# Kernel optimization log

Measured on AMD Instinct MI355X. Metric: run time of the kernel, lower is better.

## Reference

```python
import jax, jax.numpy as jnp
import numpy as np

NEG = -1.0e9


def setup_inputs() -> dict:
    key = jax.random.key(0)
    ks = jax.random.split(key, 8)
    B, L, D = 4, 2048, 1024
    s = 1.0 / np.sqrt(D)
    return {
        "x": jax.random.normal(ks[0], (B, L, D), dtype=jnp.float32),
        "Wq": jax.random.normal(ks[1], (D, D), dtype=jnp.float32) * s,
        "bq": jax.random.normal(ks[2], (D,), dtype=jnp.float32) * 0.02,
        "Wk": jax.random.normal(ks[3], (D, D), dtype=jnp.float32) * s,
        "bk": jax.random.normal(ks[4], (D,), dtype=jnp.float32) * 0.02,
        "Wv": jax.random.normal(ks[5], (D, D), dtype=jnp.float32) * s,
        "bv": jax.random.normal(ks[6], (D,), dtype=jnp.float32) * 0.02,
        "lengths": jax.random.randint(ks[7], (B,), 1, 2048, dtype=jnp.int32),
    }


def reference(x, Wq, bq, Wk, bk, Wv, bv, lengths):
    # x: [B, L, D]; single-head self-attention with causal + length additive masks
    B, L, D = x.shape
    q = x @ Wq + bq  # [B, L, D]
    k = x @ Wk + bk
    v = x @ Wv + bv
    scale = 1.0 / jnp.sqrt(jnp.asarray(D, dtype=x.dtype))
    att = jnp.einsum("bid,bjd->bij", q, k) * scale  # [B, L, L]
    idx = jnp.arange(L)
    causal = jnp.where(idx[None, :] > idx[:, None], NEG, 0.0).astype(x.dtype)  # [L, L]
    # length mask: NEG where j >= len[b] or i >= len[b]
    invalid = (idx[None, :] >= lengths[:, None])  # [B, L]
    lenmask = jnp.where(invalid[:, :, None] | invalid[:, None, :], NEG, 0.0).astype(x.dtype)
    att = att + causal[None, :, :] + lenmask
    att = jax.nn.softmax(att, axis=-1)
    return jnp.einsum("bij,bjd->bid", att, v)
```

## Files before the change

kernel.cpp:

```cpp
#include <hip/hip_runtime.h>

#define NEGV (-1.0e9f)

typedef __bf16 bf16_t;
typedef __bf16 bf16x8 __attribute__((ext_vector_type(8)));
typedef __bf16 bf16x4 __attribute__((ext_vector_type(4)));
typedef float  f32x4  __attribute__((ext_vector_type(4)));

__device__ __forceinline__ void gld16(const void* g, void* l) {
    __builtin_amdgcn_global_load_lds(
        (const __attribute__((address_space(1))) void*)g,
        (__attribute__((address_space(3))) void*)l, 16, 0, 0);
}


#define MMR(AF, IB)                                                                        \
    acc[IB][0] = __builtin_amdgcn_mfma_f32_16x16x32_bf16(AF, b0, acc[IB][0], 0, 0, 0);     \
    acc[IB][1] = __builtin_amdgcn_mfma_f32_16x16x32_bf16(AF, b1, acc[IB][1], 0, 0, 0);     \
    acc[IB][2] = __builtin_amdgcn_mfma_f32_16x16x32_bf16(AF, b2, acc[IB][2], 0, 0, 0);     \
    acc[IB][3] = __builtin_amdgcn_mfma_f32_16x16x32_bf16(AF, b3, acc[IB][3], 0, 0, 0)

__device__ __forceinline__ void ml256x256(
    const bf16_t* __restrict__ A, const bf16_t* __restrict__ B,
    int ldA, int ldB, int nkt, char* smem, int tid, f32x4 acc[8][4])
{
    const int w = tid >> 6, lane = tid & 63;
    const int wm = w & 1, wn = w >> 1;
    const int l16 = lane & 15, quad = lane >> 4;

    const int g0 = 2 * (tid >> 3) + ((tid >> 2) & 1);
    const int c0 = ((tid & 3) ^ ((tid >> 3) & 3)) * 8;
    const bf16_t* pa0 = A + (size_t)g0 * ldA + c0;
    const bf16_t* pa1 = pa0 + (size_t)128 * ldA;
    const bf16_t* pb0 = B + (size_t)g0 * ldB + c0;
    const bf16_t* pb1 = pb0 + (size_t)128 * ldB;
    char* const stA = smem + (w << 10);
    char* const stB = smem + 16384 + (w << 10);

    const int rowo = (l16 >> 1) * 128 + (l16 & 1) * 64 + ((quad ^ ((l16 >> 1) & 3)) << 4);
    const char* rdA = smem + (wm << 13) + rowo;
    const char* rdB = smem + 16384 + (wn << 12) + rowo;

#define STG6(BO) do { gld16(pa0, stA + (BO)); gld16(pa1, stA + (BO) + 8192);   \
                      gld16(pb0, stB + (BO)); gld16(pb1, stB + (BO) + 8192);   \
                      pa0 += 32; pa1 += 32; pb0 += 32; pb1 += 32; } while (0)

    STG6(0);
    if (nkt > 1) {
        STG6(32768);
        asm volatile("s_waitcnt vmcnt(4)" ::: "memory");
    } else {
        asm volatile("s_waitcnt vmcnt(0)" ::: "memory");
    }
    __builtin_amdgcn_s_barrier();

    int ro = 0, so = 65536;
    for (int kt = 0; kt < nkt; ++kt) {
        const char* ra = rdA + ro;
        const char* rb = rdB + ro;
        bf16x8 a0 = *(const bf16x8*)(ra);
        bf16x8 a1 = *(const bf16x8*)(ra + 1024);
        bf16x8 a2 = *(const bf16x8*)(ra + 2048);
        bf16x8 a3 = *(const bf16x8*)(ra + 3072);
        bf16x8 b0 = *(const bf16x8*)(rb);
        bf16x8 b1 = *(const bf16x8*)(rb + 1024);
        bf16x8 b2 = *(const bf16x8*)(rb + 2048);
        bf16x8 b3 = *(const bf16x8*)(rb + 3072);
        bf16x8 a4 = *(const bf16x8*)(ra + 4096);
        bf16x8 a5 = *(const bf16x8*)(ra + 5120);
        bf16x8 a6 = *(const bf16x8*)(ra + 6144);
        bf16x8 a7 = *(const bf16x8*)(ra + 7168);
        const bool st = (kt + 2) < nkt;
        if (st) STG6(so);
        asm volatile("s_waitcnt lgkmcnt(4)" ::: "memory");
        __builtin_amdgcn_sched_barrier(0);
        __builtin_amdgcn_s_setprio(1);
        MMR(a0, 0); MMR(a1, 1); MMR(a2, 2); MMR(a3, 3);
        __builtin_amdgcn_s_setprio(0);
        asm volatile("s_waitcnt lgkmcnt(0)" ::: "memory");
        __builtin_amdgcn_sched_barrier(0);
        __builtin_amdgcn_s_setprio(1);
        MMR(a4, 4); MMR(a5, 5); MMR(a6, 6); MMR(a7, 7);
        __builtin_amdgcn_s_setprio(0);
        if (st) asm volatile("s_waitcnt vmcnt(4)" ::: "memory");
        else    asm volatile("s_waitcnt vmcnt(0)" ::: "memory");
        __builtin_amdgcn_s_barrier();
        ro = (ro == 65536) ? 0 : (ro + 32768);
        so = (so == 65536) ? 0 : (so + 32768);
    }
#undef STG6
}

__device__ __forceinline__ void ml256x128(
    const bf16_t* __restrict__ A, const bf16_t* __restrict__ B,
    int ldA, int ldB, int nkt, char* smem, int tid, f32x4 acc[4][4])
{
    const int w = tid >> 6, lane = tid & 63;
    const int wm = w & 3, wn = w >> 2;
    const int l16 = lane & 15, quad = lane >> 4;

    const int g0 = 2 * (tid >> 3) + ((tid >> 2) & 1);
    const int c0 = ((tid & 3) ^ ((tid >> 3) & 3)) * 8;
    const bf16_t* pa0 = A + (size_t)g0 * ldA + c0;
    const bf16_t* pa1 = pa0 + (size_t)128 * ldA;
    const bf16_t* pb0 = B + (size_t)g0 * ldB + c0;
    char* const stA = smem + (w << 10);
    char* const stB = smem + 16384 + (w << 10);

    const int rowo = (l16 >> 1) * 128 + (l16 & 1) * 64 + ((quad ^ ((l16 >> 1) & 3)) << 4);
    const char* rdA = smem + (wm << 12) + rowo;
    const char* rdB = smem + 16384 + (wn << 12) + rowo;

#define STG3(BO) do { gld16(pa0, stA + (BO)); gld16(pa1, stA + (BO) + 8192);   \
                      gld16(pb0, stB + (BO));                                  \
                      pa0 += 32; pa1 += 32; pb0 += 32; } while (0)

    STG3(0);
    if (nkt > 1) {
        STG3(24576);
        asm volatile("s_waitcnt vmcnt(3)" ::: "memory");
    } else {
        asm volatile("s_waitcnt vmcnt(0)" ::: "memory");
    }
    __builtin_amdgcn_s_barrier();

    int ro = 0, so = 49152;
    for (int kt = 0; kt < nkt; ++kt) {
        const char* ra = rdA + ro;
        const char* rb = rdB + ro;
        bf16x8 a0 = *(const bf16x8*)(ra);
        bf16x8 a1 = *(const bf16x8*)(ra + 1024);
        bf16x8 a2 = *(const bf16x8*)(ra + 2048);
        bf16x8 a3 = *(const bf16x8*)(ra + 3072);
        bf16x8 b0 = *(const bf16x8*)(rb);
        bf16x8 b1 = *(const bf16x8*)(rb + 1024);
        bf16x8 b2 = *(const bf16x8*)(rb + 2048);
        bf16x8 b3 = *(const bf16x8*)(rb + 3072);
        const bool st = (kt + 2) < nkt;
        if (st) STG3(so);
        asm volatile("s_waitcnt lgkmcnt(0)" ::: "memory");
        __builtin_amdgcn_sched_barrier(0);
        __builtin_amdgcn_s_setprio(1);
        MMR(a0, 0); MMR(a1, 1); MMR(a2, 2); MMR(a3, 3);
        __builtin_amdgcn_s_setprio(0);
        if (st) asm volatile("s_waitcnt vmcnt(3)" ::: "memory");
        else    asm volatile("s_waitcnt vmcnt(0)" ::: "memory");
        __builtin_amdgcn_s_barrier();
        ro = (ro == 49152) ? 0 : (ro + 24576);
        so = (so == 49152) ? 0 : (so + 24576);
    }
#undef STG3
}

__global__ __launch_bounds__(256)
void convert_x_kernel(const float* __restrict__ x, bf16_t* __restrict__ xb)
{
    const size_t i = ((size_t)blockIdx.x * 256 + threadIdx.x) * 8;
    float4 a = *(const float4*)&x[i];
    float4 b = *(const float4*)&x[i + 4];
    bf16x8 o;
    o[0] = (bf16_t)a.x; o[1] = (bf16_t)a.y; o[2] = (bf16_t)a.z; o[3] = (bf16_t)a.w;
    o[4] = (bf16_t)b.x; o[5] = (bf16_t)b.y; o[6] = (bf16_t)b.z; o[7] = (bf16_t)b.w;
    *(bf16x8*)&xb[i] = o;
}

__global__ __launch_bounds__(256)
void transpose_w_kernel(const float* __restrict__ W0, const float* __restrict__ W1,
                        const float* __restrict__ W2, bf16_t* __restrict__ WT)
{
    __shared__ float t[32][33];
    const float* W = (blockIdx.z == 0) ? W0 : (blockIdx.z == 1) ? W1 : W2;
    bf16_t* WTz = WT + (size_t)blockIdx.z * 1024 * 1024;
    const int k0 = blockIdx.y * 32, n0 = blockIdx.x * 32;
    const int r = threadIdx.x >> 3, c4 = (threadIdx.x & 7) * 4;
    float4 v = *(const float4*)&W[(size_t)(k0 + r) * 1024 + n0 + c4];
    t[r][c4 + 0] = v.x; t[r][c4 + 1] = v.y; t[r][c4 + 2] = v.z; t[r][c4 + 3] = v.w;
    __syncthreads();
    bf16x4 o;
#pragma unroll
    for (int j = 0; j < 4; ++j) o[j] = (bf16_t)t[c4 + j][r];
    *(bf16x4*)&WTz[(size_t)(n0 + r) * 1024 + k0 + c4] = o;
}

__global__ __launch_bounds__(512, 2)
void gemm_qk256(const bf16_t* __restrict__ A, const bf16_t* __restrict__ Bt,
                const float* __restrict__ bq, const float* __restrict__ bk,
                bf16_t* __restrict__ C, int N, int Kd)
{
    __shared__ __align__(16) char smem[98304];
    int bid = blockIdx.y * 8 + blockIdx.x;
    bid = (bid & 7) * 32 + (bid >> 3);
    const int n0 = (bid & 7) * 256;
    const int m0 = (bid >> 3) * 256;
    const int tid = threadIdx.x;

    f32x4 acc[8][4];
#pragma unroll
    for (int i = 0; i < 8; ++i)
#pragma unroll
        for (int j = 0; j < 4; ++j) acc[i][j] = (f32x4)(0.0f);

    ml256x256(A + (size_t)m0 * Kd, Bt + (size_t)n0 * Kd, Kd, Kd, Kd >> 5,
              smem, tid, acc);

    const int w = tid >> 6, lane = tid & 63;
    const int wm = w & 1, wn = w >> 1, quad = lane >> 4, l16 = lane & 15;
#pragma unroll
    for (int j = 0; j < 4; ++j) {
        const int col = n0 + wn * 64 + j * 16 + l16;
        const float bval = (col < 1024) ? bq[col] : bk[col - 1024];
#pragma unroll
        for (int i = 0; i < 8; ++i) {
            const int row = m0 + wm * 128 + i * 16 + quad * 4;
#pragma unroll
            for (int r = 0; r < 4; ++r)
                C[(size_t)(row + r) * N + col] = (bf16_t)(acc[i][j][r] + bval);
        }
    }
}

__global__ __launch_bounds__(512, 2)
void gemm_vt256(const bf16_t* __restrict__ WvT, const bf16_t* __restrict__ xb,
                const float* __restrict__ bv, bf16_t* __restrict__ VT,
                int N, int Kd)
{
    __shared__ __align__(16) char smem[73728];
    int bid = blockIdx.y * 64 + blockIdx.x;
    bid = (bid & 7) * 32 + (bid >> 3);
    const int m0 = (bid >> 6) * 256;
    const int n0 = (bid & 63) * 128;
    const int tid = threadIdx.x;

    f32x4 acc[4][4];
#pragma unroll
    for (int i = 0; i < 4; ++i)
#pragma unroll
        for (int j = 0; j < 4; ++j) acc[i][j] = (f32x4)(0.0f);

    ml256x128(WvT + (size_t)m0 * Kd, xb + (size_t)n0 * Kd, Kd, Kd, Kd >> 5,
              smem, tid, acc);

    const int w = tid >> 6, lane = tid & 63;
    const int wm = w & 3, wn = w >> 2, quad = lane >> 4, l16 = lane & 15;
#pragma unroll
    for (int i = 0; i < 4; ++i) {
        const int row = m0 + wm * 64 + i * 16 + quad * 4;
#pragma unroll
        for (int r = 0; r < 4; ++r) {
            const float bval = bv[row + r];
#pragma unroll
            for (int j = 0; j < 4; ++j) {
                const int col = n0 + wn * 64 + j * 16 + l16;
                VT[(size_t)(row + r) * N + col] = (bf16_t)(acc[i][j][r] + bval);
            }
        }
    }
}

__global__ __launch_bounds__(512, 2)
void scores256(const bf16_t* __restrict__ Q, const bf16_t* __restrict__ K,
               int ldq, const int* __restrict__ lengths,
               float* __restrict__ S, int L, int Dd, float alpha)
{
    __shared__ __align__(16) char smem[98304];
    const int b = blockIdx.z;
    const int len = lengths[b];
    int it = 0;
    while ((it + 1) * (it + 2) / 2 <= (int)blockIdx.x) ++it;
    const int jt = blockIdx.x - it * (it + 1) / 2;
    const int m0 = it * 256, n0 = jt * 256;
    float* Sb = S + (size_t)b * L * L;
    const int tid = threadIdx.x;

    f32x4 acc[8][4];
#pragma unroll
    for (int i = 0; i < 8; ++i)
#pragma unroll
        for (int j = 0; j < 4; ++j) acc[i][j] = (f32x4)(0.0f);

    const bf16_t* Qb = Q + (size_t)b * L * ldq + (size_t)m0 * ldq;
    const bf16_t* Kb = K + (size_t)b * L * ldq + (size_t)n0 * ldq;
    ml256x256(Qb, Kb, ldq, ldq, Dd >> 5, smem, tid, acc);

    const int w = tid >> 6, lane = tid & 63;
    const int wm = w & 1, wn = w >> 1, quad = lane >> 4, l16 = lane & 15;
#pragma unroll
    for (int i = 0; i < 8; ++i) {
#pragma unroll
        for (int j = 0; j < 4; ++j) {
            const int col = n0 + wn * 64 + j * 16 + l16;
#pragma unroll
            for (int r = 0; r < 4; ++r) {
                const int row = m0 + wm * 128 + i * 16 + quad * 4 + r;
                float s = acc[i][j][r] * alpha;
                if (col > row) s += NEGV;
                if (row >= len || col >= len) s += NEGV;
                Sb[(size_t)row * L + col] = s;
            }
        }
    }
}

__global__ __launch_bounds__(256)
void softmax_kernel(const float* __restrict__ S, bf16_t* __restrict__ P,
                    int L, int ldp)
{
    __shared__ float red[8];
    const int i = blockIdx.x;
    const int bound  = ((i >> 7) + 1) << 7;
    const int bound2 = ((i >> 8) + 1) << 8;
    const float* row = S + ((size_t)blockIdx.y * L + i) * L;
    bf16_t* prow = P + ((size_t)blockIdx.y * L + i) * ldp;
    const int t = threadIdx.x;
    const int w = t >> 6, lane = t & 63;
    const int j8 = t * 8;
    const bool act = j8 < bound;

    float v[8];
    float m = -3.0e38f;
    if (act) {
        float4 a = *(const float4*)&row[j8];
        float4 b = *(const float4*)&row[j8 + 4];
        v[0] = a.x; v[1] = a.y; v[2] = a.z; v[3] = a.w;
        v[4] = b.x; v[5] = b.y; v[6] = b.z; v[7] = b.w;
#pragma unroll
        for (int j = 0; j < 8; ++j) m = fmaxf(m, v[j]);
    }
#pragma unroll
    for (int off = 32; off > 0; off >>= 1) m = fmaxf(m, __shfl_down(m, off, 64));
    if (lane == 0) red[w] = m;
    __syncthreads();
    m = fmaxf(fmaxf(red[0], red[1]), fmaxf(red[2], red[3]));

    float s = 0.f;
    if (act) {
#pragma unroll
        for (int j = 0; j < 8; ++j) {
            v[j] = __expf(v[j] - m);
            s += v[j];
        }
    }
#pragma unroll
    for (int off = 32; off > 0; off >>= 1) s += __shfl_down(s, off, 64);
    if (lane == 0) red[4 + w] = s;
    __syncthreads();
    s = red[4] + red[5] + red[6] + red[7];

    if (act) {
        const float inv = 1.0f / s;
        bf16x8 o;
#pragma unroll
        for (int j = 0; j < 8; ++j) o[j] = (bf16_t)(v[j] * inv);
        *(bf16x8*)&prow[j8] = o;
    } else if (j8 < bound2) {
        bf16x8 z;
#pragma unroll
        for (int j = 0; j < 8; ++j) z[j] = (bf16_t)0.0f;
        *(bf16x8*)&prow[j8] = z;
    }
}

__global__ __launch_bounds__(512, 2)
void pv256(const bf16_t* __restrict__ P, int ldp,
           const bf16_t* __restrict__ VT, int ldv,
           float* __restrict__ O, int L, int Dd)
{
    __shared__ __align__(16) char smem[73728];
    const int b = blockIdx.z;
    int bid = blockIdx.y * 8 + blockIdx.x;
    bid = (bid & 7) * 8 + (bid >> 3);
    const int mt = 7 - (bid >> 3);
    const int m0 = mt * 256, n0 = (bid & 7) * 128;
    const int tid = threadIdx.x;

    f32x4 acc[4][4];
#pragma unroll
    for (int i = 0; i < 4; ++i)
#pragma unroll
        for (int j = 0; j < 4; ++j) acc[i][j] = (f32x4)(0.0f);

    const int nkt = (m0 + 256) >> 5;
    const bf16_t* Pb = P + (size_t)b * L * ldp + (size_t)m0 * ldp;
    const bf16_t* Vb = VT + (size_t)b * L + (size_t)n0 * ldv;
    ml256x128(Pb, Vb, ldp, ldv, nkt, smem, tid, acc);

    float* Ob = O + (size_t)b * L * Dd;
    const int w = tid >> 6, lane = tid & 63;
    const int wm = w & 3, wn = w >> 2, quad = lane >> 4, l16 = lane & 15;
#pragma unroll
    for (int i = 0; i < 4; ++i) {
        const int row = m0 + wm * 64 + i * 16 + quad * 4;
#pragma unroll
        for (int j = 0; j < 4; ++j) {
            const int col = n0 + wn * 64 + j * 16 + l16;
#pragma unroll
            for (int r = 0; r < 4; ++r)
                Ob[(size_t)(row + r) * Dd + col] = acc[i][j][r];
        }
    }
}

extern "C" void kernel_launch(void* const* d_in, const int* in_sizes, int n_in,
                              void* d_out, int out_size, void* d_ws, size_t ws_size,
                              hipStream_t stream)
{
    const float* x  = (const float*)d_in[0];
    const float* Wq = (const float*)d_in[1];
    const float* bq = (const float*)d_in[2];
    const float* Wk = (const float*)d_in[3];
    const float* bk = (const float*)d_in[4];
    const float* Wv = (const float*)d_in[5];
    const float* bv = (const float*)d_in[6];
    const int*  len = (const int*)d_in[7];
    float* out = (float*)d_out;

    const int B = 4, L = 2048, D = 1024;
    const int M = B * L;
    const int N2 = 2 * D;

    bf16_t* xb = (bf16_t*)d_ws;
    bf16_t* WT = xb + (size_t)M * D;
    bf16_t* QK = WT + (size_t)3 * D * D;
    bf16_t* VT = QK + (size_t)M * N2;
    float*  S  = (float*)(VT + (size_t)D * M);
    bf16_t* P  = QK;

    convert_x_kernel<<<(M * D) / 2048, 256, 0, stream>>>(x, xb);

    transpose_w_kernel<<<dim3(32, 32, 3), 256, 0, stream>>>(Wq, Wk, Wv, WT);

    gemm_qk256<<<dim3(8, 32), 512, 0, stream>>>(xb, WT, bq, bk, QK, N2, D);

    gemm_vt256<<<dim3(64, 4), 512, 0, stream>>>(
        WT + (size_t)2 * D * D, xb, bv, VT, M, D);

    scores256<<<dim3(36, 1, B), 512, 0, stream>>>(
        QK, QK + 1024, N2, len, S, L, D, 0.03125f);

    softmax_kernel<<<dim3(L, B), 256, 0, stream>>>(S, P, L, N2);

    pv256<<<dim3(8, 8, 4), 512, 0, stream>>>(P, N2, VT, M, out, L, D);
}
```

Before: 244.0 us.

## Fuse partial softmax into scores epilogue and rescale P chunks in PV load

The scores kernel now computes per-64-column chunk max and exp-sum in its epilogue and stores unnormalized exponentials as bf16 instead of fp32 logits. A small finalize kernel combines the chunk statistics into per-chunk scale factors. The PV kernel loads U through registers, multiplies each element by its chunk scale, and writes it to LDS. This replaces the full softmax pass over an fp32 LxL matrix and halves score storage traffic, at the cost of register-staged A loads in the PV pipeline instead of direct global-to-LDS loads, plus added epilogue shuffles.

```diff
diff --git a/kernel.cpp b/kernel.cpp
--- a/kernel.cpp
+++ b/kernel.cpp
@@ -152,6 +152,94 @@
 #undef STG3
 }
 
+__device__ __forceinline__ bf16x8 scale8(bf16x8 u, float c) {
+    bf16x8 o;
+#pragma unroll
+    for (int j = 0; j < 8; ++j) o[j] = (bf16_t)((float)u[j] * c);
+    return o;
+}
+
+__device__ __forceinline__ void ml_pv(
+    const bf16_t* __restrict__ A, const float* __restrict__ scA,
+    const bf16_t* __restrict__ B,
+    int ldA, int ldB, int nkt, char* smem, int tid, f32x4 acc[4][4])
+{
+    const int w = tid >> 6, lane = tid & 63;
+    const int wm = w & 3, wn = w >> 2;
+    const int l16 = lane & 15, quad = lane >> 4;
+
+    const int g0 = 2 * (tid >> 3) + ((tid >> 2) & 1);
+    const int c0 = ((tid & 3) ^ ((tid >> 3) & 3)) * 8;
+    const bf16_t* pa0 = A + (size_t)g0 * ldA + c0;
+    const bf16_t* pa1 = pa0 + (size_t)128 * ldA;
+    const bf16_t* pb0 = B + (size_t)g0 * ldB + c0;
+    const float* sc0 = scA + g0 * 32;
+    const float* sc1 = sc0 + 128 * 32;
+
+    char* const stB = smem + 16384 + (w << 10);
+    char* const wA0 = smem + tid * 16;
+    char* const wA1 = smem + 8192 + tid * 16;
+
+    const int rowo = (l16 >> 1) * 128 + (l16 & 1) * 64 + ((quad ^ ((l16 >> 1) & 3)) << 4);
+    const char* rdA = smem + (wm << 12) + rowo;
+    const char* rdB = smem + 16384 + (wn << 12) + rowo;
+
+    {
+        bf16x8 x00 = *(const bf16x8*)(pa0);
+        bf16x8 x01 = *(const bf16x8*)(pa1);
+        bf16x8 x10 = *(const bf16x8*)(pa0 + 32);
+        bf16x8 x11 = *(const bf16x8*)(pa1 + 32);
+        gld16(pb0, stB + 0);     pb0 += 32;
+        gld16(pb0, stB + 24576); pb0 += 32;
+        const float c00 = sc0[c0 >> 6],        c01 = sc1[c0 >> 6];
+        const float c10 = sc0[(32 + c0) >> 6], c11 = sc1[(32 + c0) >> 6];
+        *(bf16x8*)(wA0)         = scale8(x00, c00);
+        *(bf16x8*)(wA1)         = scale8(x01, c01);
+        *(bf16x8*)(wA0 + 24576) = scale8(x10, c10);
+        *(bf16x8*)(wA1 + 24576) = scale8(x11, c11);
+        asm volatile("s_waitcnt vmcnt(0) lgkmcnt(0)" ::: "memory");
+        __builtin_amdgcn_s_barrier();
+    }
+
+    int ro = 0, so = 49152;
+    for (int kt = 0; kt < nkt; ++kt) {
+        const bool st = (kt + 2) < nkt;
+        bf16x8 x0, x1; float ca0 = 0.f, ca1 = 0.f;
+        if (st) {
+            x0 = *(const bf16x8*)(pa0 + (size_t)(kt + 2) * 32);
+            x1 = *(const bf16x8*)(pa1 + (size_t)(kt + 2) * 32);
+            const int ch = ((kt + 2) * 32 + c0) >> 6;
+            ca0 = sc0[ch]; ca1 = sc1[ch];
+            gld16(pb0, stB + so); pb0 += 32;
+        }
+        const char* ra = rdA + ro;
+        const char* rb = rdB + ro;
+        bf16x8 a0 = *(const bf16x8*)(ra);
+        bf16x8 a1 = *(const bf16x8*)(ra + 1024);
+        bf16x8 a2 = *(const bf16x8*)(ra + 2048);
+        bf16x8 a3 = *(const bf16x8*)(ra + 3072);
+        bf16x8 b0 = *(const bf16x8*)(rb);
+        bf16x8 b1 = *(const bf16x8*)(rb + 1024);
+        bf16x8 b2 = *(const bf16x8*)(rb + 2048);
+        bf16x8 b3 = *(const bf16x8*)(rb + 3072);
+        asm volatile("s_waitcnt lgkmcnt(0)" ::: "memory");
+        __builtin_amdgcn_sched_barrier(0);
+        __builtin_amdgcn_s_setprio(1);
+        MMR(a0, 0); MMR(a1, 1); MMR(a2, 2); MMR(a3, 3);
+        __builtin_amdgcn_s_setprio(0);
+        if (st) {
+            *(bf16x8*)(wA0 + so) = scale8(x0, ca0);
+            *(bf16x8*)(wA1 + so) = scale8(x1, ca1);
+        } else {
+            asm volatile("s_waitcnt vmcnt(0)" ::: "memory");
+        }
+        asm volatile("s_waitcnt lgkmcnt(0)" ::: "memory");
+        __builtin_amdgcn_s_barrier();
+        ro = (ro == 49152) ? 0 : (ro + 24576);
+        so = (so == 49152) ? 0 : (so + 24576);
+    }
+}
+
 __global__ __launch_bounds__(256)
 void convert_x_kernel(const float* __restrict__ x, bf16_t* __restrict__ xb)
 {
@@ -260,7 +348,8 @@
 __global__ __launch_bounds__(512, 2)
 void scores256(const bf16_t* __restrict__ Q, const bf16_t* __restrict__ K,
                int ldq, const int* __restrict__ lengths,
-               float* __restrict__ S, int L, int Dd, float alpha)
+               bf16_t* __restrict__ U, float2* __restrict__ stats,
+               int L, int Dd, float alpha)
 {
     __shared__ __align__(16) char smem[98304];
     const int b = blockIdx.z;
@@ -269,7 +358,6 @@
     while ((it + 1) * (it + 2) / 2 <= (int)blockIdx.x) ++it;
     const int jt = blockIdx.x - it * (it + 1) / 2;
     const int m0 = it * 256, n0 = jt * 256;
-    float* Sb = S + (size_t)b * L * L;
     const int tid = threadIdx.x;
 
     f32x4 acc[8][4];
@@ -284,84 +372,74 @@
 
     const int w = tid >> 6, lane = tid & 63;
     const int wm = w & 1, wn = w >> 1, quad = lane >> 4, l16 = lane & 15;
+    bf16_t* Ub = U + (size_t)b * L * L;
+    float2* strow = stats + (size_t)b * L * 32;
+    const int chnk = (n0 >> 6) + wn;
 #pragma unroll
     for (int i = 0; i < 8; ++i) {
 #pragma unroll
-        for (int j = 0; j < 4; ++j) {
-            const int col = n0 + wn * 64 + j * 16 + l16;
-#pragma unroll
-            for (int r = 0; r < 4; ++r) {
-                const int row = m0 + wm * 128 + i * 16 + quad * 4 + r;
-                float s = acc[i][j][r] * alpha;
-                if (col > row) s += NEGV;
-                if (row >= len || col >= len) s += NEGV;
-                Sb[(size_t)row * L + col] = s;
+        for (int r = 0; r < 4; ++r) {
+            const int row = m0 + wm * 128 + i * 16 + quad * 4 + r;
+            float sv[4];
+#pragma unroll
+            for (int j = 0; j < 4; ++j) {
+                const int col = n0 + wn * 64 + j * 16 + l16;
+                float v = acc[i][j][r] * alpha;
+                if (col > row) v += NEGV;
+                if (row >= len || col >= len) v += NEGV;
+                sv[j] = v;
             }
+            float m = fmaxf(fmaxf(sv[0], sv[1]), fmaxf(sv[2], sv[3]));
+            m = fmaxf(m, __shfl_xor(m, 1, 64));
+            m = fmaxf(m, __shfl_xor(m, 2, 64));
+            m = fmaxf(m, __shfl_xor(m, 4, 64));
+            m = fmaxf(m, __shfl_xor(m, 8, 64));
+            float ssum = 0.f;
+#pragma unroll
+            for (int j = 0; j < 4; ++j) {
+                sv[j] = __expf(sv[j] - m);
+                ssum += sv[j];
+            }
+            ssum += __shfl_xor(ssum, 1, 64);
+            ssum += __shfl_xor(ssum, 2, 64);
+            ssum += __shfl_xor(ssum, 4, 64);
+            ssum += __shfl_xor(ssum, 8, 64);
+#pragma unroll
+            for (int j = 0; j < 4; ++j)
+                Ub[(size_t)row * L + n0 + wn * 64 + j * 16 + l16] = (bf16_t)sv[j];
+            if (l16 == 0) strow[(size_t)row * 32 + chnk] = make_float2(m, ssum);
         }
     }
 }
 
 __global__ __launch_bounds__(256)
-void softmax_kernel(const float* __restrict__ S, bf16_t* __restrict__ P,
-                    int L, int ldp)
-{
-    __shared__ float red[8];
-    const int i = blockIdx.x;
-    const int bound  = ((i >> 7) + 1) << 7;
-    const int bound2 = ((i >> 8) + 1) << 8;
-    const float* row = S + ((size_t)blockIdx.y * L + i) * L;
-    bf16_t* prow = P + ((size_t)blockIdx.y * L + i) * ldp;
+void sm_finalize(const float2* __restrict__ stats, float* __restrict__ scale, int L)
+{
     const int t = threadIdx.x;
-    const int w = t >> 6, lane = t & 63;
-    const int j8 = t * 8;
-    const bool act = j8 < bound;
-
-    float v[8];
-    float m = -3.0e38f;
-    if (act) {
-        float4 a = *(const float4*)&row[j8];
-        float4 b = *(const float4*)&row[j8 + 4];
-        v[0] = a.x; v[1] = a.y; v[2] = a.z; v[3] = a.w;
-        v[4] = b.x; v[5] = b.y; v[6] = b.z; v[7] = b.w;
-#pragma unroll
-        for (int j = 0; j < 8; ++j) m = fmaxf(m, v[j]);
-    }
-#pragma unroll
-    for (int off = 32; off > 0; off >>= 1) m = fmaxf(m, __shfl_down(m, off, 64));
-    if (lane == 0) red[w] = m;
-    __syncthreads();
-    m = fmaxf(fmaxf(red[0], red[1]), fmaxf(red[2], red[3]));
-
-    float s = 0.f;
-    if (act) {
-#pragma unroll
-        for (int j = 0; j < 8; ++j) {
-            v[j] = __expf(v[j] - m);
-            s += v[j];
-        }
-    }
-#pragma unroll
-    for (int off = 32; off > 0; off >>= 1) s += __shfl_down(s, off, 64);
-    if (lane == 0) red[4 + w] = s;
-    __syncthreads();
-    s = red[4] + red[5] + red[6] + red[7];
-
-    if (act) {
-        const float inv = 1.0f / s;
-        bf16x8 o;
-#pragma unroll
-        for (int j = 0; j < 8; ++j) o[j] = (bf16_t)(v[j] * inv);
-        *(bf16x8*)&prow[j8] = o;
-    } else if (j8 < bound2) {
-        bf16x8 z;
-#pragma unroll
-        for (int j = 0; j < 8; ++j) z[j] = (bf16_t)0.0f;
-        *(bf16x8*)&prow[j8] = z;
-    }
+    const int c = t & 31;
+    const int row = blockIdx.x * 8 + (t >> 5);
+    const size_t base = ((size_t)blockIdx.y * L + row) * 32;
+    const int nch = ((row >> 8) + 1) << 2;
+    float m_c = -3.0e38f, s_c = 0.f;
+    if (c < nch) { float2 st = stats[base + c]; m_c = st.x; s_c = st.y; }
+    float M = m_c;
+    M = fmaxf(M, __shfl_xor(M, 1, 64));
+    M = fmaxf(M, __shfl_xor(M, 2, 64));
+    M = fmaxf(M, __shfl_xor(M, 4, 64));
+    M = fmaxf(M, __shfl_xor(M, 8, 64));
+    M = fmaxf(M, __shfl_xor(M, 16, 64));
+    const float e = __expf(m_c - M);
+    float d = s_c * e;
+    d += __shfl_xor(d, 1, 64);
+    d += __shfl_xor(d, 2, 64);
+    d += __shfl_xor(d, 4, 64);
+    d += __shfl_xor(d, 8, 64);
+    d += __shfl_xor(d, 16, 64);
+    if (c < nch) scale[base + c] = e / d;
 }
 
 __global__ __launch_bounds__(512, 2)
-void pv256(const bf16_t* __restrict__ P, int ldp,
+void pv256(const bf16_t* __restrict__ U, int ldp, const float* __restrict__ scale,
            const bf16_t* __restrict__ VT, int ldv,
            float* __restrict__ O, int L, int Dd)
 {
@@ -380,9 +458,10 @@
         for (int j = 0; j < 4; ++j) acc[i][j] = (f32x4)(0.0f);
 
     const int nkt = (m0 + 256) >> 5;
-    const bf16_t* Pb = P + (size_t)b * L * ldp + (size_t)m0 * ldp;
+    const bf16_t* Pb = U + (size_t)b * L * ldp + (size_t)m0 * ldp;
+    const float* scA = scale + ((size_t)b * L + m0) * 32;
     const bf16_t* Vb = VT + (size_t)b * L + (size_t)n0 * ldv;
-    ml256x128(Pb, Vb, ldp, ldv, nkt, smem, tid, acc);
+    ml_pv(Pb, scA, Vb, ldp, ldv, nkt, smem, tid, acc);
 
     float* Ob = O + (size_t)b * L * Dd;
     const int w = tid >> 6, lane = tid & 63;
@@ -422,8 +501,9 @@
     bf16_t* WT = xb + (size_t)M * D;
     bf16_t* QK = WT + (size_t)3 * D * D;
     bf16_t* VT = QK + (size_t)M * N2;
-    float*  S  = (float*)(VT + (size_t)D * M);
-    bf16_t* P  = QK;
+    bf16_t* U  = VT + (size_t)D * M;
+    float2* stats = (float2*)(U + (size_t)B * L * L);
+    float*  scale = (float*)(stats + (size_t)B * L * 32);
 
     convert_x_kernel<<<(M * D) / 2048, 256, 0, stream>>>(x, xb);
 
@@ -435,9 +515,9 @@
         WT + (size_t)2 * D * D, xb, bv, VT, M, D);
 
     scores256<<<dim3(36, 1, B), 512, 0, stream>>>(
-        QK, QK + 1024, N2, len, S, L, D, 0.03125f);
-
-    softmax_kernel<<<dim3(L, B), 256, 0, stream>>>(S, P, L, N2);
-
-    pv256<<<dim3(8, 8, 4), 512, 0, stream>>>(P, N2, VT, M, out, L, D);
-}
+        QK, QK + 1024, N2, len, U, stats, L, D, 0.03125f);
+
+    sm_finalize<<<dim3(L / 8, B), 256, 0, stream>>>(stats, scale, L);
+
+    pv256<<<dim3(8, 8, 4), 512, 0, stream>>>(U, L, scale, VT, M, out, L, D);
+}
```

After: 275.4 us. 1.13x slower.

## Fuse partial softmax into scores kernel, store bf16 exps with per-chunk stats

Applied to the files above, without the earlier changes.

The scores kernel now computes per-row, per-64-column-chunk max and exp-sum in registers and writes unnormalized bf16 exponentials plus float2 stats, instead of writing fp32 scores. A small finalize kernel combines the chunk stats into per-chunk scale factors and rescales the bf16 row in place before the PV GEMM reads it. This halves score-matrix traffic and removes the separate max and sum passes over fp32 data. In exchange it adds an extra bf16 rounding before rescaling, and P now lives in a new buffer with leading dimension L instead of reusing the QK buffer.

```diff
diff --git a/kernel.cpp b/kernel.cpp
--- a/kernel.cpp
+++ b/kernel.cpp
@@ -260,7 +260,8 @@
 __global__ __launch_bounds__(512, 2)
 void scores256(const bf16_t* __restrict__ Q, const bf16_t* __restrict__ K,
                int ldq, const int* __restrict__ lengths,
-               float* __restrict__ S, int L, int Dd, float alpha)
+               bf16_t* __restrict__ U, float2* __restrict__ stats,
+               int L, int Dd, float alpha)
 {
     __shared__ __align__(16) char smem[98304];
     const int b = blockIdx.z;
@@ -269,7 +270,6 @@
     while ((it + 1) * (it + 2) / 2 <= (int)blockIdx.x) ++it;
     const int jt = blockIdx.x - it * (it + 1) / 2;
     const int m0 = it * 256, n0 = jt * 256;
-    float* Sb = S + (size_t)b * L * L;
     const int tid = threadIdx.x;
 
     f32x4 acc[8][4];
@@ -284,79 +284,86 @@
 
     const int w = tid >> 6, lane = tid & 63;
     const int wm = w & 1, wn = w >> 1, quad = lane >> 4, l16 = lane & 15;
+    bf16_t* Ub = U + (size_t)b * L * L;
+    float2* strow = stats + (size_t)b * L * 32;
+    const int chnk = (n0 >> 6) + wn;
 #pragma unroll
     for (int i = 0; i < 8; ++i) {
 #pragma unroll
-        for (int j = 0; j < 4; ++j) {
-            const int col = n0 + wn * 64 + j * 16 + l16;
-#pragma unroll
-            for (int r = 0; r < 4; ++r) {
-                const int row = m0 + wm * 128 + i * 16 + quad * 4 + r;
-                float s = acc[i][j][r] * alpha;
-                if (col > row) s += NEGV;
-                if (row >= len || col >= len) s += NEGV;
-                Sb[(size_t)row * L + col] = s;
+        for (int r = 0; r < 4; ++r) {
+            const int row = m0 + wm * 128 + i * 16 + quad * 4 + r;
+            float sv[4];
+#pragma unroll
+            for (int j = 0; j < 4; ++j) {
+                const int col = n0 + wn * 64 + j * 16 + l16;
+                float v = acc[i][j][r] * alpha;
+                if (col > row) v += NEGV;
+                if (row >= len || col >= len) v += NEGV;
+                sv[j] = v;
             }
+            float m = fmaxf(fmaxf(sv[0], sv[1]), fmaxf(sv[2], sv[3]));
+            m = fmaxf(m, __shfl_xor(m, 1, 64));
+            m = fmaxf(m, __shfl_xor(m, 2, 64));
+            m = fmaxf(m, __shfl_xor(m, 4, 64));
+            m = fmaxf(m, __shfl_xor(m, 8, 64));
+            float ssum = 0.f;
+#pragma unroll
+            for (int j = 0; j < 4; ++j) {
+                sv[j] = __expf(sv[j] - m);
+                ssum += sv[j];
+            }
+            ssum += __shfl_xor(ssum, 1, 64);
+            ssum += __shfl_xor(ssum, 2, 64);
+            ssum += __shfl_xor(ssum, 4, 64);
+            ssum += __shfl_xor(ssum, 8, 64);
+#pragma unroll
+            for (int j = 0; j < 4; ++j)
+                Ub[(size_t)row * L + n0 + wn * 64 + j * 16 + l16] = (bf16_t)sv[j];
+            if (l16 == 0) strow[(size_t)row * 32 + chnk] = make_float2(m, ssum);
         }
     }
 }
 
 __global__ __launch_bounds__(256)
-void softmax_kernel(const float* __restrict__ S, bf16_t* __restrict__ P,
-                    int L, int ldp)
-{
-    __shared__ float red[8];
+void sm_finalize_norm(const float2* __restrict__ stats, bf16_t* __restrict__ U,
+                      int L)
+{
+    __shared__ float sc[32];
     const int i = blockIdx.x;
-    const int bound  = ((i >> 7) + 1) << 7;
     const int bound2 = ((i >> 8) + 1) << 8;
-    const float* row = S + ((size_t)blockIdx.y * L + i) * L;
-    bf16_t* prow = P + ((size_t)blockIdx.y * L + i) * ldp;
+    const int nch = bound2 >> 6;
+    const size_t base = ((size_t)blockIdx.y * L + i) * 32;
     const int t = threadIdx.x;
-    const int w = t >> 6, lane = t & 63;
+
+    if (t < 32) {
+        float m_c = -3.0e38f, s_c = 0.f;
+        if (t < nch) { float2 st = stats[base + t]; m_c = st.x; s_c = st.y; }
+        float M = m_c;
+        M = fmaxf(M, __shfl_xor(M, 1, 64));
+        M = fmaxf(M, __shfl_xor(M, 2, 64));
+        M = fmaxf(M, __shfl_xor(M, 4, 64));
+        M = fmaxf(M, __shfl_xor(M, 8, 64));
+        M = fmaxf(M, __shfl_xor(M, 16, 64));
+        const float e = __expf(m_c - M);
+        float d = s_c * e;
+        d += __shfl_xor(d, 1, 64);
+        d += __shfl_xor(d, 2, 64);
+        d += __shfl_xor(d, 4, 64);
+        d += __shfl_xor(d, 8, 64);
+        d += __shfl_xor(d, 16, 64);
+        sc[t] = e / d;
+    }
+    __syncthreads();
+
     const int j8 = t * 8;
-    const bool act = j8 < bound;
-
-    float v[8];
-    float m = -3.0e38f;
-    if (act) {
-        float4 a = *(const float4*)&row[j8];
-        float4 b = *(const float4*)&row[j8 + 4];
-        v[0] = a.x; v[1] = a.y; v[2] = a.z; v[3] = a.w;
-        v[4] = b.x; v[5] = b.y; v[6] = b.z; v[7] = b.w;
-#pragma unroll
-        for (int j = 0; j < 8; ++j) m = fmaxf(m, v[j]);
-    }
-#pragma unroll
-    for (int off = 32; off > 0; off >>= 1) m = fmaxf(m, __shfl_down(m, off, 64));
-    if (lane == 0) red[w] = m;
-    __syncthreads();
-    m = fmaxf(fmaxf(red[0], red[1]), fmaxf(red[2], red[3]));
-
-    float s = 0.f;
-    if (act) {
-#pragma unroll
-        for (int j = 0; j < 8; ++j) {
-            v[j] = __expf(v[j] - m);
-            s += v[j];
-        }
-    }
-#pragma unroll
-    for (int off = 32; off > 0; off >>= 1) s += __shfl_down(s, off, 64);
-    if (lane == 0) red[4 + w] = s;
-    __syncthreads();
-    s = red[4] + red[5] + red[6] + red[7];
-
-    if (act) {
-        const float inv = 1.0f / s;
+    if (j8 < bound2) {
+        bf16_t* row = U + ((size_t)blockIdx.y * L + i) * L;
+        bf16x8 u = *(const bf16x8*)&row[j8];
+        const float c = sc[t >> 3];
         bf16x8 o;
 #pragma unroll
-        for (int j = 0; j < 8; ++j) o[j] = (bf16_t)(v[j] * inv);
-        *(bf16x8*)&prow[j8] = o;
-    } else if (j8 < bound2) {
-        bf16x8 z;
-#pragma unroll
-        for (int j = 0; j < 8; ++j) z[j] = (bf16_t)0.0f;
-        *(bf16x8*)&prow[j8] = z;
+        for (int j = 0; j < 8; ++j) o[j] = (bf16_t)((float)u[j] * c);
+        *(bf16x8*)&row[j8] = o;
     }
 }
 
@@ -422,8 +429,8 @@
     bf16_t* WT = xb + (size_t)M * D;
     bf16_t* QK = WT + (size_t)3 * D * D;
     bf16_t* VT = QK + (size_t)M * N2;
-    float*  S  = (float*)(VT + (size_t)D * M);
-    bf16_t* P  = QK;
+    bf16_t* U  = VT + (size_t)D * M;
+    float2* stats = (float2*)(U + (size_t)B * L * L);
 
     convert_x_kernel<<<(M * D) / 2048, 256, 0, stream>>>(x, xb);
 
@@ -435,9 +442,9 @@
         WT + (size_t)2 * D * D, xb, bv, VT, M, D);
 
     scores256<<<dim3(36, 1, B), 512, 0, stream>>>(
-        QK, QK + 1024, N2, len, S, L, D, 0.03125f);
-
-    softmax_kernel<<<dim3(L, B), 256, 0, stream>>>(S, P, L, N2);
-
-    pv256<<<dim3(8, 8, 4), 512, 0, stream>>>(P, N2, VT, M, out, L, D);
-}
+        QK, QK + 1024, N2, len, U, stats, L, D, 0.03125f);
+
+    sm_finalize_norm<<<dim3(L, B), 256, 0, stream>>>(stats, U, L);
+
+    pv256<<<dim3(8, 8, 4), 512, 0, stream>>>(U, L, VT, M, out, L, D);
+}
```

New measurement: 246.2 us. About the same (+0.9%).
